# Optimization experiments

Measured on AMD Instinct MI355X. Metric: run time of the kernel, lower is better.

The kernel has to match this reference:

```python
import jax, jax.numpy as jnp
import numpy as np

TRIANGLE_TABLE = np.array([
    [-1, -1, -1, -1, -1, -1], [1, 0, 2, -1, -1, -1], [4, 0, 3, -1, -1, -1], [1, 4, 2, 1, 3, 4],
    [3, 1, 5, -1, -1, -1], [2, 3, 0, 2, 5, 3], [1, 4, 0, 1, 5, 4], [4, 2, 5, -1, -1, -1],
    [4, 5, 2, -1, -1, -1], [4, 1, 0, 4, 5, 1], [3, 2, 0, 3, 5, 2], [1, 3, 5, -1, -1, -1],
    [4, 1, 2, 4, 3, 1], [3, 0, 4, -1, -1, -1], [2, 0, 1, -1, -1, -1], [-1, -1, -1, -1, -1, -1]], np.int32)
NUM_TRIANGLES_TABLE = np.array([0, 1, 1, 2, 1, 2, 2, 1, 1, 2, 2, 1, 2, 1, 1, 0], np.int32)
BASE_TET_EDGES = np.array([0, 1, 0, 2, 0, 3, 1, 2, 1, 3, 2, 3], np.int32)


def _make_tet_grid(R):
    # Regular grid in [0,1]^3, each cube split into 6 tets along the 0-7 diagonal.
    r1 = R + 1
    gi, gj, gk = np.meshgrid(np.arange(r1), np.arange(r1), np.arange(r1), indexing='ij')
    verts = (np.stack([gi, gj, gk], -1).reshape(-1, 3) / R).astype(np.float32)  # (Nv,3)
    ci, cj, ck = np.meshgrid(np.arange(R), np.arange(R), np.arange(R), indexing='ij')
    ci, cj, ck = ci.ravel(), cj.ravel(), ck.ravel()
    def vid(dx, dy, dz):
        return ((ci + dx) * r1 + (cj + dy)) * r1 + (ck + dz)
    corners = [vid((c >> 2) & 1, (c >> 1) & 1, c & 1) for c in range(8)]
    tet_corners = [(0, 1, 3, 7), (0, 3, 2, 7), (0, 2, 6, 7), (0, 6, 4, 7), (0, 4, 5, 7), (0, 5, 1, 7)]
    tets = np.stack([np.stack([corners[a] for a in t], -1) for t in tet_corners], 1).reshape(-1, 4)
    return verts, tets.astype(np.int32)


def setup_inputs() -> dict:
    R = 64
    verts, tets = _make_tet_grid(R)
    key = jax.random.key(0)
    k1, k2 = jax.random.split(key)
    level = jax.random.normal(k1, (verts.shape[0],), dtype=jnp.float32)
    deformation = jax.random.normal(k2, (verts.shape[0], 3), dtype=jnp.float32)
    return {
        'level': level,
        'deformation': deformation,
        'grid_vertices': jnp.asarray(verts),
        'tet_indices': jnp.asarray(tets),
        'resolution': R,
    }


def reference(level, deformation, grid_vertices, tet_indices, resolution):
    # normalize_grid_deformation: (range_hi - range_lo)/res * tanh(offsets), range = (0,1)
    pos = grid_vertices + jnp.tanh(deformation) / resolution  # (Nv,3)
    occ = level > 0                                           # (Nv,)
    occ_f = occ[tet_indices]                                  # (F,4)
    occ_sum = occ_f.sum(-1)
    valid = (occ_sum > 0) & (occ_sum < 4)
    vt = tet_indices[valid]                                   # (Fv,4)
    occ_valid = occ_f[valid]                                  # (Fv,4)
    # per-tet edges, each sorted (min,max) -> dedup
    edges = vt[:, jnp.asarray(BASE_TET_EDGES)].reshape(-1, 2)  # (6*Fv,2)
    edges = jnp.sort(edges, axis=1)
    unique_edges, idx_map = jnp.unique(edges, axis=0, return_inverse=True)
    idx_map = idx_map.reshape(-1)
    # edges that actually cross the isosurface (exactly one endpoint inside)
    mask_edges = occ[unique_edges].sum(-1) == 1               # (U,)
    mapping = jnp.where(mask_edges, jnp.cumsum(mask_edges.astype(jnp.int32)) - 1, -1)
    idx_map = mapping[idx_map].reshape(-1, 6)                 # (Fv,6)
    interp_v = unique_edges[mask_edges]                       # (M,2)
    # linear interpolation of crossing point along each edge
    ep = pos[interp_v]                                        # (M,2,3)
    es = level[interp_v] * jnp.array([1.0, -1.0], dtype=level.dtype)  # (M,2) = [sdf0, -sdf1]
    w = es[:, ::-1] / es.sum(1, keepdims=True)                # (M,2) = [-sdf1, sdf0]/(sdf0-sdf1)
    verts_out = (ep * w[:, :, None]).sum(1)                   # (M,3)
    # triangle table lookup
    v_id = jnp.array([1, 2, 4, 8], dtype=jnp.int32)
    tetindex = (occ_valid.astype(jnp.int32) * v_id).sum(-1)   # (Fv,)
    tri_tab = jnp.asarray(TRIANGLE_TABLE)
    num_tri = jnp.asarray(NUM_TRIANGLES_TABLE)[tetindex]
    m1 = num_tri == 1
    m2 = num_tri == 2
    f1 = jnp.take_along_axis(idx_map[m1], tri_tab[tetindex[m1]][:, :3], axis=1).reshape(-1, 3)
    f2 = jnp.take_along_axis(idx_map[m2], tri_tab[tetindex[m2]][:, :6], axis=1).reshape(-1, 3)
    faces = jnp.concatenate([f1, f2], axis=0)                 # (Nf,3)
    return verts_out, faces
```

## Files before the change

### kernel.cpp

```cpp
#include <hip/hip_runtime.h>
#include <math.h>


typedef unsigned long long ull;

#define ST_LD(p)    __hip_atomic_load((p), __ATOMIC_RELAXED, __HIP_MEMORY_SCOPE_AGENT)
#define ST_ST(p,v)  __hip_atomic_store((p), (v), __ATOMIC_RELAXED, __HIP_MEMORY_SCOPE_AGENT)

__device__ __forceinline__ float fast_tanh(float x) {
    float e = __expf(2.0f * x);
    return __fdividef(e - 1.0f, e + 1.0f);
}

__device__ __constant__ int c_tri_tab[16][6] = {
    {-1,-1,-1,-1,-1,-1},{1,0,2,-1,-1,-1},{4,0,3,-1,-1,-1},{1,4,2,1,3,4},
    {3,1,5,-1,-1,-1},{2,3,0,2,5,3},{1,4,0,1,5,4},{4,2,5,-1,-1,-1},
    {4,5,2,-1,-1,-1},{4,1,0,4,5,1},{3,2,0,3,5,2},{1,3,5,-1,-1,-1},
    {4,1,2,4,3,1},{3,0,4,-1,-1,-1},{2,0,1,-1,-1,-1},{-1,-1,-1,-1,-1,-1}};
__device__ __constant__ int c_num_tri[16] = {0,1,1,2,1,2,2,1,1,2,2,1,2,1,1,0};
__device__ __constant__ int c_tc[6][4] = {{0,1,3,7},{0,3,2,7},{0,2,6,7},{0,6,4,7},{0,4,5,7},{0,5,1,7}};
__device__ __constant__ int c_te[6][6] = {
    {(0<<3)|0,(0<<3)|2,(0<<3)|6,(1<<3)|1,(1<<3)|5,(3<<3)|3},
    {(0<<3)|2,(0<<3)|1,(0<<3)|6,(2<<3)|0,(3<<3)|3,(2<<3)|4},
    {(0<<3)|1,(0<<3)|5,(0<<3)|6,(2<<3)|3,(2<<3)|4,(6<<3)|0},
    {(0<<3)|5,(0<<3)|3,(0<<3)|6,(4<<3)|1,(6<<3)|0,(4<<3)|2},
    {(0<<3)|3,(0<<3)|4,(0<<3)|6,(4<<3)|0,(4<<3)|2,(5<<3)|1},
    {(0<<3)|4,(0<<3)|0,(0<<3)|6,(1<<3)|3,(5<<3)|1,(1<<3)|5}};

#define TAG      (1ull << 62)
#define PMASK    ((1ull << 60) - 1ull)
#define READY(s) (((s) >> 62) == 1ull)

__global__ void k_vert(const float* __restrict__ level, const float* __restrict__ deform,
                       int NV, int r1, float invR,
                       ull* __restrict__ stateA, ull* __restrict__ prefS,
                       unsigned* __restrict__ rankWord, unsigned char* __restrict__ obByte,
                       uint2* __restrict__ cubeRank, int* __restrict__ totals,
                       float* __restrict__ out) {
    int b = blockIdx.x;
    int v = b * 256 + threadIdx.x;
    int R = r1 - 1, rsq = r1 * r1;
    bool valid = v < NV;
    float la = valid ? level[v] : 0.f;
    bool occv = valid && (la > 0.f);

    int x = 0, y = 0, z = 0, flags = 0, n1 = 0, n2 = 0, cidx = 0;
    bool interior = false;
    float lb[7];
    if (valid) {
        x = v / rsq; int rem = v - x * rsq; y = rem / r1; z = rem - y * r1;
        bool bx = x < R, by = y < R, bz = z < R;
        interior = bx && by && bz;
        bool inb[7] = {bz, by, by && bz, bx, bx && bz, bx && by, interior};
        int deltas[7] = {1, r1, r1 + 1, rsq, rsq + 1, rsq + r1, rsq + r1 + 1};
        int ob = occv ? 1 : 0;
        for (int j = 0; j < 7; j++) {
            float l = inb[j] ? level[v + deltas[j]] : 0.f;
            lb[j] = l;
            bool o = inb[j] && (l > 0.f);
            ob |= (o ? 1 : 0) << (j + 1);
            if (inb[j] && (o != occv)) flags |= 1 << j;
        }
        if (interior) {
            cidx = ((x * R) + y) * R + z;
            obByte[cidx] = (unsigned char)ob;
            for (int k = 0; k < 6; k++) {
                int ti = ((ob >> c_tc[k][0]) & 1) | (((ob >> c_tc[k][1]) & 1) << 1)
                       | (((ob >> c_tc[k][2]) & 1) << 2) | (((ob >> c_tc[k][3]) & 1) << 3);
                int n = c_num_tri[ti];
                n1 += (n == 1); n2 += (n == 2);
            }
        }
    }
    int cnt = __popc(flags);
    int pk = n1 | (n2 << 16);
    int lane = threadIdx.x & 63, wv = threadIdx.x >> 6;
    int inclE = cnt, inclT = pk;
    for (int o = 1; o < 64; o <<= 1) {
        int tE = __shfl_up(inclE, o);
        int tT = __shfl_up(inclT, o);
        if (lane >= o) { inclE += tE; inclT += tT; }
    }
    __shared__ int wE[4], wT[4];
    __shared__ ull sExcl;
    if (lane == 63) { wE[wv] = inclE; wT[wv] = inclT; }
    __syncthreads();

    if (wv == 0) {
        int eb = 0, t1b = 0, t2b = 0;
        if (lane == 0) {
            eb = wE[0] + wE[1] + wE[2] + wE[3];
            int tb = wT[0] + wT[1] + wT[2] + wT[3];
            t1b = tb & 0xffff; t2b = tb >> 16;
            ST_ST(&stateA[b], TAG | ((ull)eb << 40) | ((ull)t1b << 20) | (ull)t2b);
        }
        ull sum = 0;
        for (int w = 0; 64 * w < b; w++) {
            int i = b - 1 - 64 * w - lane;
            ull pv = (i >= 0) ? ST_LD(&prefS[i]) : 0;
            ull pm = __ballot(i >= 0 && READY(pv));
            int Lp = pm ? (__ffsll((long long)pm) - 1) : 64;
            ull val = 0;
            if (i >= 0 && lane < Lp) {
                ull s;
                do { s = ST_LD(&stateA[i]); } while (!READY(s));
                val = s & PMASK;
            } else if (i >= 0 && lane == Lp) {
                val = pv & PMASK;
            }
            for (int o = 1; o < 64; o <<= 1) val += __shfl_xor(val, o);
            sum += val;
            if (Lp < 64) break;
        }
        if (lane == 0) {
            sExcl = sum;
            ull inc = sum + (((ull)eb << 40) | ((ull)t1b << 20) | (ull)t2b);
            ST_ST(&prefS[b], TAG | inc);
            if (b == (int)gridDim.x - 1) {
                totals[0] = (int)((inc >> 40) & 0xFFFFF);
                totals[1] = (int)((inc >> 20) & 0xFFFFF);
                totals[2] = (int)(inc & 0xFFFFF);
            }
        }
    }
    __syncthreads();

    ull ex = sExcl;
    int exclE = (int)((ex >> 40) & 0xFFFFF);
    int excl1 = (int)((ex >> 20) & 0xFFFFF);
    int excl2 = (int)(ex & 0xFFFFF);
    int woffE = 0, woffT = 0;
    for (int w = 0; w < wv; w++) { woffE += wE[w]; woffT += wT[w]; }
    int rank0 = exclE + woffE + inclE - cnt;
    int tExcl = woffT + inclT - pk;
    if (interior)
        cubeRank[cidx] = make_uint2((unsigned)(excl1 + (tExcl & 0xffff)),
                                    (unsigned)(excl2 + (tExcl >> 16)));

    if (valid)
        rankWord[v] = (unsigned)rank0 | ((unsigned)flags << 21);

    if (flags) {
        int deltas[7] = {1, r1, r1 + 1, rsq, rsq + 1, rsq + r1, rsq + r1 + 1};
        const int dxs[7] = {0, 0, 0, 1, 1, 1, 1};
        const int dys[7] = {0, 1, 1, 0, 0, 1, 1};
        const int dzs[7] = {1, 0, 1, 0, 1, 0, 1};
        float pax = x * invR + fast_tanh(deform[3 * v])     * invR;
        float pay = y * invR + fast_tanh(deform[3 * v + 1]) * invR;
        float paz = z * invR + fast_tanh(deform[3 * v + 2]) * invR;
        int r = rank0;
        for (int j = 0; j < 7; j++) {
            if (!((flags >> j) & 1)) continue;
            int bb = v + deltas[j];
            float lbv = lb[j];
            float inv = __fdividef(1.0f, la - lbv);
            float w0 = -lbv * inv;
            float w1f = la * inv;
            float pbx = (x + dxs[j]) * invR + fast_tanh(deform[3 * bb])     * invR;
            float pby = (y + dys[j]) * invR + fast_tanh(deform[3 * bb + 1]) * invR;
            float pbz = (z + dzs[j]) * invR + fast_tanh(deform[3 * bb + 2]) * invR;
            out[3 * r]     = pax * w0 + pbx * w1f;
            out[3 * r + 1] = pay * w0 + pby * w1f;
            out[3 * r + 2] = paz * w0 + pbz * w1f;
            r++;
        }
    }
}

__global__ void k_face(int NV, int r1, int NT,
                       const unsigned char* __restrict__ obByte,
                       const uint2* __restrict__ cubeRank,
                       const unsigned* __restrict__ rankWord, const int* __restrict__ totals,
                       float* __restrict__ out) {
    __shared__ ull tab[256];
    if (threadIdx.x < 256) {
        int ob = threadIdx.x;
        ull w = 0;
        for (int k = 0; k < 6; k++) {
            int ti = ((ob >> c_tc[k][0]) & 1) | (((ob >> c_tc[k][1]) & 1) << 1)
                   | (((ob >> c_tc[k][2]) & 1) << 2) | (((ob >> c_tc[k][3]) & 1) << 3);
            w |= (ull)ti << (4 * k);
            w |= (ull)c_num_tri[ti] << (32 + 2 * k);
        }
        tab[ob] = w;
    }
    __syncthreads();

    int t = blockIdx.x * 256 + threadIdx.x;
    if (t >= NT) return;
    int c = t / 6;
    int k = t - c * 6;
    int ob = obByte[c];
    ull w = tab[ob];
    int nt = (int)(w >> (32 + 2 * k)) & 3;
    if (nt == 0) return;
    int ti = (int)(w >> (4 * k)) & 15;
    int pre1 = 0, pre2 = 0;
    for (int kk = 0; kk < k; kk++) {
        int m = (int)(w >> (32 + 2 * kk)) & 3;
        pre1 += (m == 1); pre2 += (m == 2);
    }
    uint2 cr = cubeRank[c];
    int R = r1 - 1, rsq = r1 * r1;
    int rr = R * R;
    int cx = c / rr; int rem = c - cx * rr; int cy = rem / R; int cz = rem - cy * R;
    int v = (cx * r1 + cy) * r1 + cz;

    int M = totals[0], N1 = totals[1];
    float* faces = out + 3 * (size_t)M;
    int off[8] = {0, 1, r1, r1 + 1, rsq, rsq + 1, rsq + r1, rsq + r1 + 1};
    int ne = nt * 3;
    float vals[6];
    for (int e = 0; e < ne; e++) {
        int le = c_tri_tab[ti][e];
        int ce = c_te[k][le];
        int a = v + off[ce >> 3];
        int j = ce & 7;
        unsigned rw = rankWord[a];
        int rk = (int)(rw & 0x1FFFFF) + __popc((rw >> 21) & (unsigned)((1 << j) - 1));
        vals[e] = (float)rk;
    }
    if (nt == 1) {
        size_t base = 3 * (size_t)(cr.x + pre1);
        faces[base] = vals[0]; faces[base + 1] = vals[1]; faces[base + 2] = vals[2];
    } else {
        size_t base = 3 * ((size_t)N1 + 2 * (size_t)(cr.y + pre2));
        for (int e = 0; e < 6; e++) faces[base + e] = vals[e];
    }
}

extern "C" void kernel_launch(void* const* d_in, const int* in_sizes, int n_in,
                              void* d_out, int out_size, void* d_ws, size_t ws_size,
                              hipStream_t stream) {
    const float* level  = (const float*)d_in[0];
    const float* deform = (const float*)d_in[1];
    int NV = in_sizes[0];
    int r1 = 1;
    while ((long long)r1 * r1 * r1 < (long long)NV) r1++;
    int R = r1 - 1;
    float invR = 1.0f / (float)R;

    int nb = (NV + 255) / 256;
    int NC = R * R * R;
    int NT = 6 * NC;
    int nbT = (NT + 255) / 256;

    char* w = (char*)d_ws;
    unsigned* rankWord = (unsigned*)w;
    w += (((size_t)NV * sizeof(unsigned)) + 255) & ~(size_t)255;
    unsigned char* obByte = (unsigned char*)w;
    w += (((size_t)NC) + 255) & ~(size_t)255;
    uint2* cubeRank = (uint2*)w;
    w += (((size_t)NC * 8) + 255) & ~(size_t)255;
    ull* stateA = (ull*)w;
    ull* prefS = stateA + nb;
    int* totals = (int*)(prefS + nb);

    float* out = (float*)d_out;

    k_vert<<<nb, 256, 0, stream>>>(level, deform, NV, r1, invR, stateA, prefS,
                                   rankWord, obByte, cubeRank, totals, out);
    k_face<<<nbT, 256, 0, stream>>>(NV, r1, NT, obByte, cubeRank, rankWord, totals, out);
}
```

Measured before the change: 130.2 us.

## Replace decoupled look-back scan with reduce-scan-propagate passes and pack cube info

```diff
diff --git a/kernel.cpp b/kernel.cpp
--- a/kernel.cpp
+++ b/kernel.cpp
@@ -3,9 +3,6 @@
 
 
 typedef unsigned long long ull;
-
-#define ST_LD(p)    __hip_atomic_load((p), __ATOMIC_RELAXED, __HIP_MEMORY_SCOPE_AGENT)
-#define ST_ST(p,v)  __hip_atomic_store((p), (v), __ATOMIC_RELAXED, __HIP_MEMORY_SCOPE_AGENT)
 
 __device__ __forceinline__ float fast_tanh(float x) {
     float e = __expf(2.0f * x);
@@ -27,15 +24,93 @@
     {(0<<3)|3,(0<<3)|4,(0<<3)|6,(4<<3)|0,(4<<3)|2,(5<<3)|1},
     {(0<<3)|4,(0<<3)|0,(0<<3)|6,(1<<3)|3,(5<<3)|1,(1<<3)|5}};
 
-#define TAG      (1ull << 62)
-#define PMASK    ((1ull << 60) - 1ull)
-#define READY(s) (((s) >> 62) == 1ull)
+__global__ void k_reduce(const float* __restrict__ level, int NV, int r1,
+                         ull* __restrict__ stateA) {
+    int b = blockIdx.x;
+    int v = b * 256 + threadIdx.x;
+    int R = r1 - 1, rsq = r1 * r1;
+    bool valid = v < NV;
+    float la = valid ? level[v] : 0.f;
+    bool occv = valid && (la > 0.f);
+
+    int flags = 0, n1 = 0, n2 = 0;
+    if (valid) {
+        int x = v / rsq; int rem = v - x * rsq; int y = rem / r1; int z = rem - y * r1;
+        bool bx = x < R, by = y < R, bz = z < R;
+        bool interior = bx && by && bz;
+        bool inb[7] = {bz, by, by && bz, bx, bx && bz, bx && by, interior};
+        int deltas[7] = {1, r1, r1 + 1, rsq, rsq + 1, rsq + r1, rsq + r1 + 1};
+        int ob = occv ? 1 : 0;
+        for (int j = 0; j < 7; j++) {
+            float l = inb[j] ? level[v + deltas[j]] : 0.f;
+            bool o = inb[j] && (l > 0.f);
+            ob |= (o ? 1 : 0) << (j + 1);
+            if (inb[j] && (o != occv)) flags |= 1 << j;
+        }
+        if (interior) {
+            for (int k = 0; k < 6; k++) {
+                int ti = ((ob >> c_tc[k][0]) & 1) | (((ob >> c_tc[k][1]) & 1) << 1)
+                       | (((ob >> c_tc[k][2]) & 1) << 2) | (((ob >> c_tc[k][3]) & 1) << 3);
+                int n = c_num_tri[ti];
+                n1 += (n == 1); n2 += (n == 2);
+            }
+        }
+    }
+    int cnt = __popc(flags);
+    int pk = n1 | (n2 << 16);
+    for (int o = 1; o < 64; o <<= 1) { cnt += __shfl_xor(cnt, o); pk += __shfl_xor(pk, o); }
+    __shared__ int sE[4], sT[4];
+    int lane = threadIdx.x & 63, wv = threadIdx.x >> 6;
+    if (lane == 0) { sE[wv] = cnt; sT[wv] = pk; }
+    __syncthreads();
+    if (threadIdx.x == 0) {
+        int eb = sE[0] + sE[1] + sE[2] + sE[3];
+        int tb = sT[0] + sT[1] + sT[2] + sT[3];
+        stateA[b] = ((ull)eb << 40) | ((ull)(tb & 0xffff) << 20) | (ull)(tb >> 16);
+    }
+}
+
+__global__ __launch_bounds__(1024) void k_scan(int nb, const ull* __restrict__ stateA,
+                                               ull* __restrict__ prefS,
+                                               int* __restrict__ totals) {
+    __shared__ ull wTot[16], wOff[16];
+    __shared__ ull carrySh;
+    int tid = threadIdx.x, lane = tid & 63, wv = tid >> 6;
+    ull carry = 0;
+    int rounds = (nb + 1023) >> 10;
+    for (int r = 0; r < rounds; r++) {
+        int i = (r << 10) + tid;
+        ull a = (i < nb) ? stateA[i] : 0ull;
+        ull incl = a;
+        for (int o = 1; o < 64; o <<= 1) {
+            ull t = (ull)__shfl_up((long long)incl, o);
+            if (lane >= o) incl += t;
+        }
+        if (lane == 63) wTot[wv] = incl;
+        __syncthreads();
+        if (tid == 0) {
+            ull s = 0;
+            for (int k = 0; k < 16; k++) { ull t = wTot[k]; wOff[k] = s; s += t; }
+            carrySh = s;
+        }
+        __syncthreads();
+        ull excl = carry + wOff[wv] + (incl - a);
+        if (i < nb) prefS[i] = excl;
+        if (i == nb - 1) {
+            ull inc = excl + a;
+            totals[0] = (int)((inc >> 40) & 0xFFFFF);
+            totals[1] = (int)((inc >> 20) & 0xFFFFF);
+            totals[2] = (int)(inc & 0xFFFFF);
+        }
+        carry += carrySh;
+        __syncthreads();
+    }
+}
 
 __global__ void k_vert(const float* __restrict__ level, const float* __restrict__ deform,
                        int NV, int r1, float invR,
-                       ull* __restrict__ stateA, ull* __restrict__ prefS,
-                       unsigned* __restrict__ rankWord, unsigned char* __restrict__ obByte,
-                       uint2* __restrict__ cubeRank, int* __restrict__ totals,
+                       const ull* __restrict__ prefS,
+                       unsigned* __restrict__ rankWord, ull* __restrict__ cubeInfo,
                        float* __restrict__ out) {
     int b = blockIdx.x;
     int v = b * 256 + threadIdx.x;
@@ -44,7 +119,7 @@
     float la = valid ? level[v] : 0.f;
     bool occv = valid && (la > 0.f);
 
-    int x = 0, y = 0, z = 0, flags = 0, n1 = 0, n2 = 0, cidx = 0;
+    int x = 0, y = 0, z = 0, flags = 0, n1 = 0, n2 = 0, cidx = 0, ob = 0;
     bool interior = false;
     float lb[7];
     if (valid) {
@@ -53,7 +128,7 @@
         interior = bx && by && bz;
         bool inb[7] = {bz, by, by && bz, bx, bx && bz, bx && by, interior};
         int deltas[7] = {1, r1, r1 + 1, rsq, rsq + 1, rsq + r1, rsq + r1 + 1};
-        int ob = occv ? 1 : 0;
+        ob = occv ? 1 : 0;
         for (int j = 0; j < 7; j++) {
             float l = inb[j] ? level[v + deltas[j]] : 0.f;
             lb[j] = l;
@@ -63,7 +138,6 @@
         }
         if (interior) {
             cidx = ((x * R) + y) * R + z;
-            obByte[cidx] = (unsigned char)ob;
             for (int k = 0; k < 6; k++) {
                 int ti = ((ob >> c_tc[k][0]) & 1) | (((ob >> c_tc[k][1]) & 1) << 1)
                        | (((ob >> c_tc[k][2]) & 1) << 2) | (((ob >> c_tc[k][3]) & 1) << 3);
@@ -82,61 +156,21 @@
         if (lane >= o) { inclE += tE; inclT += tT; }
     }
     __shared__ int wE[4], wT[4];
-    __shared__ ull sExcl;
     if (lane == 63) { wE[wv] = inclE; wT[wv] = inclT; }
     __syncthreads();
 
-    if (wv == 0) {
-        int eb = 0, t1b = 0, t2b = 0;
-        if (lane == 0) {
-            eb = wE[0] + wE[1] + wE[2] + wE[3];
-            int tb = wT[0] + wT[1] + wT[2] + wT[3];
-            t1b = tb & 0xffff; t2b = tb >> 16;
-            ST_ST(&stateA[b], TAG | ((ull)eb << 40) | ((ull)t1b << 20) | (ull)t2b);
-        }
-        ull sum = 0;
-        for (int w = 0; 64 * w < b; w++) {
-            int i = b - 1 - 64 * w - lane;
-            ull pv = (i >= 0) ? ST_LD(&prefS[i]) : 0;
-            ull pm = __ballot(i >= 0 && READY(pv));
-            int Lp = pm ? (__ffsll((long long)pm) - 1) : 64;
-            ull val = 0;
-            if (i >= 0 && lane < Lp) {
-                ull s;
-                do { s = ST_LD(&stateA[i]); } while (!READY(s));
-                val = s & PMASK;
-            } else if (i >= 0 && lane == Lp) {
-                val = pv & PMASK;
-            }
-            for (int o = 1; o < 64; o <<= 1) val += __shfl_xor(val, o);
-            sum += val;
-            if (Lp < 64) break;
-        }
-        if (lane == 0) {
-            sExcl = sum;
-            ull inc = sum + (((ull)eb << 40) | ((ull)t1b << 20) | (ull)t2b);
-            ST_ST(&prefS[b], TAG | inc);
-            if (b == (int)gridDim.x - 1) {
-                totals[0] = (int)((inc >> 40) & 0xFFFFF);
-                totals[1] = (int)((inc >> 20) & 0xFFFFF);
-                totals[2] = (int)(inc & 0xFFFFF);
-            }
-        }
-    }
-    __syncthreads();
-
-    ull ex = sExcl;
+    ull ex = prefS[b];
     int exclE = (int)((ex >> 40) & 0xFFFFF);
     int excl1 = (int)((ex >> 20) & 0xFFFFF);
     int excl2 = (int)(ex & 0xFFFFF);
     int woffE = 0, woffT = 0;
-    for (int w = 0; w < wv; w++) { woffE += wE[w]; woffT += wT[w]; }
+    for (int w2 = 0; w2 < wv; w2++) { woffE += wE[w2]; woffT += wT[w2]; }
     int rank0 = exclE + woffE + inclE - cnt;
     int tExcl = woffT + inclT - pk;
     if (interior)
-        cubeRank[cidx] = make_uint2((unsigned)(excl1 + (tExcl & 0xffff)),
-                                    (unsigned)(excl2 + (tExcl >> 16)));
-
+        cubeInfo[cidx] = (ull)(unsigned)ob
+                       | ((ull)(unsigned)(excl1 + (tExcl & 0xffff)) << 8)
+                       | ((ull)(unsigned)(excl2 + (tExcl >> 16)) << 28);
     if (valid)
         rankWord[v] = (unsigned)rank0 | ((unsigned)flags << 21);
 
@@ -167,22 +201,31 @@
     }
 }
 
-__global__ void k_face(int NV, int r1, int NT,
-                       const unsigned char* __restrict__ obByte,
-                       const uint2* __restrict__ cubeRank,
-                       const unsigned* __restrict__ rankWord, const int* __restrict__ totals,
+__global__ void k_face(int r1, int NT,
+                       const ull* __restrict__ cubeInfo,
+                       const unsigned* __restrict__ rankWord,
+                       const int* __restrict__ totals,
                        float* __restrict__ out) {
-    __shared__ ull tab[256];
-    if (threadIdx.x < 256) {
-        int ob = threadIdx.x;
-        ull w = 0;
-        for (int k = 0; k < 6; k++) {
-            int ti = ((ob >> c_tc[k][0]) & 1) | (((ob >> c_tc[k][1]) & 1) << 1)
-                   | (((ob >> c_tc[k][2]) & 1) << 2) | (((ob >> c_tc[k][3]) & 1) << 3);
-            w |= (ull)ti << (4 * k);
-            w |= (ull)c_num_tri[ti] << (32 + 2 * k);
-        }
-        tab[ob] = w;
+    __shared__ ull tab[1536];
+    for (int idx = threadIdx.x; idx < 1536; idx += 256) {
+        int ob = idx & 255, k = idx >> 8;
+        int ti = ((ob >> c_tc[k][0]) & 1) | (((ob >> c_tc[k][1]) & 1) << 1)
+               | (((ob >> c_tc[k][2]) & 1) << 2) | (((ob >> c_tc[k][3]) & 1) << 3);
+        int nt = c_num_tri[ti];
+        int pre1 = 0, pre2 = 0;
+        for (int kk = 0; kk < k; kk++) {
+            int tik = ((ob >> c_tc[kk][0]) & 1) | (((ob >> c_tc[kk][1]) & 1) << 1)
+                    | (((ob >> c_tc[kk][2]) & 1) << 2) | (((ob >> c_tc[kk][3]) & 1) << 3);
+            int m = c_num_tri[tik];
+            pre1 += (m == 1); pre2 += (m == 2);
+        }
+        ull w = (ull)nt | ((ull)pre1 << 2) | ((ull)pre2 << 5);
+        for (int e = 0; e < 6; e++) {
+            int le = c_tri_tab[ti][e];
+            int ce = (le >= 0) ? c_te[k][le] : 0;
+            w |= (ull)ce << (8 + 6 * e);
+        }
+        tab[idx] = w;
     }
     __syncthreads();
 
@@ -190,43 +233,39 @@
     if (t >= NT) return;
     int c = t / 6;
     int k = t - c * 6;
-    int ob = obByte[c];
-    ull w = tab[ob];
-    int nt = (int)(w >> (32 + 2 * k)) & 3;
+    ull info = cubeInfo[c];
+    ull w = tab[(k << 8) + ((int)info & 255)];
+    int nt = (int)w & 3;
     if (nt == 0) return;
-    int ti = (int)(w >> (4 * k)) & 15;
-    int pre1 = 0, pre2 = 0;
-    for (int kk = 0; kk < k; kk++) {
-        int m = (int)(w >> (32 + 2 * kk)) & 3;
-        pre1 += (m == 1); pre2 += (m == 2);
-    }
-    uint2 cr = cubeRank[c];
-    int R = r1 - 1, rsq = r1 * r1;
-    int rr = R * R;
+
+    int rsq = r1 * r1, R = r1 - 1, rr = R * R;
     int cx = c / rr; int rem = c - cx * rr; int cy = rem / R; int cz = rem - cy * R;
     int v = (cx * r1 + cy) * r1 + cz;
-
     int M = totals[0], N1 = totals[1];
     float* faces = out + 3 * (size_t)M;
-    int off[8] = {0, 1, r1, r1 + 1, rsq, rsq + 1, rsq + r1, rsq + r1 + 1};
-    int ne = nt * 3;
-    float vals[6];
-    for (int e = 0; e < ne; e++) {
-        int le = c_tri_tab[ti][e];
-        int ce = c_te[k][le];
-        int a = v + off[ce >> 3];
-        int j = ce & 7;
-        unsigned rw = rankWord[a];
-        int rk = (int)(rw & 0x1FFFFF) + __popc((rw >> 21) & (unsigned)((1 << j) - 1));
-        vals[e] = (float)rk;
-    }
+    ull we = w >> 8;
+
+    #define ERANK(ce_)                                                          \
+        ({ int ce = (ce_);                                                      \
+           int a = v + ((ce >> 5) & 1) * rsq + ((ce >> 4) & 1) * r1 + ((ce >> 3) & 1); \
+           unsigned rw = rankWord[a];                                           \
+           (float)((int)(rw & 0x1FFFFF) + __popc((rw >> 21) & ((1u << (ce & 7)) - 1u))); })
+
     if (nt == 1) {
-        size_t base = 3 * (size_t)(cr.x + pre1);
-        faces[base] = vals[0]; faces[base + 1] = vals[1]; faces[base + 2] = vals[2];
+        unsigned r1c = (unsigned)(info >> 8) & 0xFFFFF;
+        int pre1 = ((int)w >> 2) & 7;
+        size_t base = 3 * (size_t)(r1c + pre1);
+        faces[base]     = ERANK((int)(we) & 63);
+        faces[base + 1] = ERANK((int)(we >> 6) & 63);
+        faces[base + 2] = ERANK((int)(we >> 12) & 63);
     } else {
-        size_t base = 3 * ((size_t)N1 + 2 * (size_t)(cr.y + pre2));
-        for (int e = 0; e < 6; e++) faces[base + e] = vals[e];
-    }
+        unsigned r2c = (unsigned)(info >> 28) & 0xFFFFF;
+        int pre2 = ((int)w >> 5) & 7;
+        size_t base = 3 * ((size_t)N1 + 2 * (size_t)(r2c + pre2));
+        #pragma unroll
+        for (int e = 0; e < 6; e++) faces[base + e] = ERANK((int)(we >> (6 * e)) & 63);
+    }
+    #undef ERANK
 }
 
 extern "C" void kernel_launch(void* const* d_in, const int* in_sizes, int n_in,
@@ -248,17 +287,19 @@
     char* w = (char*)d_ws;
     unsigned* rankWord = (unsigned*)w;
     w += (((size_t)NV * sizeof(unsigned)) + 255) & ~(size_t)255;
-    unsigned char* obByte = (unsigned char*)w;
-    w += (((size_t)NC) + 255) & ~(size_t)255;
-    uint2* cubeRank = (uint2*)w;
+    ull* cubeInfo = (ull*)w;
     w += (((size_t)NC * 8) + 255) & ~(size_t)255;
     ull* stateA = (ull*)w;
-    ull* prefS = stateA + nb;
-    int* totals = (int*)(prefS + nb);
+    w += (((size_t)nb * 8) + 255) & ~(size_t)255;
+    ull* prefS = (ull*)w;
+    w += (((size_t)nb * 8) + 255) & ~(size_t)255;
+    int* totals = (int*)w;
 
     float* out = (float*)d_out;
 
-    k_vert<<<nb, 256, 0, stream>>>(level, deform, NV, r1, invR, stateA, prefS,
-                                   rankWord, obByte, cubeRank, totals, out);
-    k_face<<<nbT, 256, 0, stream>>>(NV, r1, NT, obByte, cubeRank, rankWord, totals, out);
-}
+    k_reduce<<<nb, 256, 0, stream>>>(level, NV, r1, stateA);
+    k_scan<<<1, 1024, 0, stream>>>(nb, stateA, prefS, totals);
+    k_vert<<<nb, 256, 0, stream>>>(level, deform, NV, r1, invR, prefS,
+                                   rankWord, cubeInfo, out);
+    k_face<<<nbT, 256, 0, stream>>>(r1, NT, cubeInfo, rankWord, totals, out);
+}
```

After: 170.7 us. 1.31x slower.
